# Performance work log

Hardware: AMD Instinct MI355X
Metric: run time of the kernel (lower is better)

The kernel has to match this reference:

```python
import jax, jax.numpy as jnp
import numpy as np

HEADS = 16
DIM_HEAD = 64
SCALE = DIM_HEAD ** -0.5
MASK_NEG = 1000000.0


def setup_inputs() -> dict:
    key = jax.random.key(0)
    ks = jax.random.split(key, 6)
    B, N, M, D = 2, 2048, 2048, 1024
    inner = HEADS * DIM_HEAD  # 1024
    x = jax.random.normal(ks[0], (B, N, D), dtype=jnp.float32)
    context = jax.random.normal(ks[1], (B, M, D), dtype=jnp.float32)
    mask = jax.random.randint(ks[2], (B, N), 0, 2, dtype=jnp.int32)
    Wq = jax.random.normal(ks[3], (D, inner), dtype=jnp.float32) * (D ** -0.5)
    Wkv = jax.random.normal(ks[4], (D, 2 * inner), dtype=jnp.float32) * (D ** -0.5)
    Wout = jax.random.normal(ks[5], (inner, D), dtype=jnp.float32) * (inner ** -0.5)
    bout = jnp.zeros((D,), dtype=jnp.float32)
    return {"x": x, "context": context, "mask": mask,
            "Wq": Wq, "Wkv": Wkv, "Wout": Wout, "bout": bout}


def _split_heads(t):
    # [b, n, (h d)] -> [b, h, n, d]
    b, n, _ = t.shape
    return t.reshape(b, n, HEADS, DIM_HEAD).transpose(0, 2, 1, 3)


def reference(x, context, mask, Wq, Wkv, Wout, bout):
    kv = context @ Wkv                      # [b, m, 2*inner]
    k, v = jnp.split(kv, 2, axis=-1)
    q = x @ Wq                              # [b, n, inner]
    q, k, v = _split_heads(q), _split_heads(k), _split_heads(v)
    dots = jnp.einsum('bhnd,bhmd->bhnm', q, k) * SCALE
    # mask is [b, n]: additive penalty per query row (faithful to source)
    dots = dots - (1.0 - mask.astype(jnp.float32))[:, None, :, None] * MASK_NEG
    attn = jax.nn.softmax(dots, axis=-1)
    out = jnp.einsum('bhnm,bhmd->bhnd', attn, v)  # [b, h, n, d]
    b, h, n, d = out.shape
    out = out.transpose(0, 2, 1, 3).reshape(b, n, h * d)
    return out @ Wout + bout
```

## Files before the change

### kernel.cpp

```cpp
#include <hip/hip_runtime.h>
#include <hip/hip_bf16.h>
#include <math.h>

#define BATCH   2
#define NQ      2048
#define NKV     2048
#define DMODEL  1024
#define HEADS   16
#define INNER   1024
#define KVCOLS  2048

typedef short bf16x8 __attribute__((ext_vector_type(8)));
typedef float f32x4  __attribute__((ext_vector_type(4)));

__device__ __forceinline__ short f2bf(float x) {
    __hip_bfloat16 h = __float2bfloat16(x);
    return *reinterpret_cast<short*>(&h);
}
__device__ __forceinline__ float bf2f(short h) {
    unsigned int u = ((unsigned int)(unsigned short)h) << 16;
    float f;
    __builtin_memcpy(&f, &u, 4);
    return f;
}
__device__ __forceinline__ void gl_lds16(const void* g, void* l) {
    __builtin_amdgcn_global_load_lds(
        (const __attribute__((address_space(1))) unsigned int*)g,
        (__attribute__((address_space(3))) unsigned int*)l, 16, 0, 0);
}
__device__ __forceinline__ int sw(int row, int chunk) {
    return row * 64 + ((chunk ^ (row & 7)) << 3);
}

__device__ __forceinline__ void split_chunk(const float* __restrict__ in,
                                            short* __restrict__ hi,
                                            short* __restrict__ lo, int id)
{
    const int i = (id * 256 + (int)threadIdx.x) * 4;
    float4 v = *(const float4*)(in + i);
    short4 h, l;
    h.x = f2bf(v.x); l.x = f2bf(v.x - bf2f(h.x));
    h.y = f2bf(v.y); l.y = f2bf(v.y - bf2f(h.y));
    h.z = f2bf(v.z); l.z = f2bf(v.z - bf2f(h.z));
    h.w = f2bf(v.w); l.w = f2bf(v.w - bf2f(h.w));
    *(short4*)(hi + i) = h;
    *(short4*)(lo + i) = l;
}

__device__ __forceinline__ void tile_transpose_split(
    const float* __restrict__ W, short* __restrict__ Wth, short* __restrict__ Wtl,
    int Kd, int Nd, int bx, int by, int split)
{
    __shared__ float t[32][33];
    const int lx = threadIdx.x & 31, ly = threadIdx.x >> 5;
    #pragma unroll
    for (int j = 0; j < 4; ++j)
        t[ly + j * 8][lx] = W[(size_t)(by * 32 + ly + j * 8) * Nd + bx * 32 + lx];
    __syncthreads();
    #pragma unroll
    for (int j = 0; j < 4; ++j) {
        const float v = t[lx][ly + j * 8];
        const short h = f2bf(v);
        const size_t idx = (size_t)(bx * 32 + ly + j * 8) * Kd + by * 32 + lx;
        Wth[idx] = h;
        if (split) Wtl[idx] = f2bf(v - bf2f(h));
    }
}

__global__ __launch_bounds__(256)
void prep_all(const float* __restrict__ x, const float* __restrict__ ctx,
              const float* __restrict__ Wq, const float* __restrict__ Wkv,
              const float* __restrict__ Wout,
              short* __restrict__ xh, short* __restrict__ xl,
              short* __restrict__ ch, short* __restrict__ cl,
              short* __restrict__ WqTh, short* __restrict__ WqTl,
              short* __restrict__ WkvTh, short* __restrict__ WkvTl,
              short* __restrict__ WoutT)
{
    const int id = blockIdx.x;
    if (id < 4096) {
        split_chunk(x, xh, xl, id);
    } else if (id < 8192) {
        split_chunk(ctx, ch, cl, id - 4096);
    } else {
        const int r = id - 8192;
        if (r < 1024)
            tile_transpose_split(Wq, WqTh, WqTl, 1024, 1024, r & 31, r >> 5, 1);
        else if (r < 3072)
            tile_transpose_split(Wkv, WkvTh, WkvTl, 1024, 2048, (r - 1024) & 63, (r - 1024) >> 6, 1);
        else
            tile_transpose_split(Wout, WoutT, nullptr, 1024, 1024, (r - 3072) & 31, (r - 3072) >> 5, 0);
    }
}

__global__ __launch_bounds__(256)
void qkv_gemm(const short* __restrict__ xh, const short* __restrict__ xl,
              const short* __restrict__ ch, const short* __restrict__ cl,
              const short* __restrict__ WqTh, const short* __restrict__ WqTl,
              const short* __restrict__ WkvTh, const short* __restrict__ WkvTl,
              short* __restrict__ qhp, short* __restrict__ qlp,
              short* __restrict__ khp, short* __restrict__ klp,
              short* __restrict__ vp)
{
    __shared__ short Ash[128 * 32];
    __shared__ short Asl[128 * 32];
    __shared__ short Bsh[128 * 32];
    __shared__ short Bsl[128 * 32];

    const int tid = threadIdx.x;
    const int z = blockIdx.z;
    const int m0 = blockIdx.y * 128, n0 = blockIdx.x * 128;
    const int w = tid >> 6, ln = tid & 63;
    const int wm = (w & 1) * 64, wn = (w >> 1) * 64;
    const int lr = ln & 15, lq = ln >> 4;
    const int terms = (z == 2) ? 1 : 3;

    const short* Ah  = (z == 0) ? xh : ch;
    const short* Al  = (z == 0) ? xl : cl;
    const short* Bth = (z == 0) ? WqTh : (z == 1 ? WkvTh : WkvTh + (size_t)1024 * 1024);
    const short* Btl = (z == 0) ? WqTl : WkvTl;

    f32x4 acc[4][4];
    #pragma unroll
    for (int mt = 0; mt < 4; ++mt)
        #pragma unroll
        for (int nt = 0; nt < 4; ++nt)
            #pragma unroll
            for (int r = 0; r < 4; ++r) acc[mt][nt][r] = 0.0f;

    for (int k0 = 0; k0 < 1024; k0 += 32) {
        __syncthreads();
        #pragma unroll
        for (int it = 0; it < 2; ++it) {
            const int f = it * 256 + tid;
            const int row = f >> 2, c = f & 3;
            const int cg = c ^ ((row >> 1) & 3);
            const size_t ao = (size_t)(m0 + row) * 1024 + k0 + cg * 8;
            const size_t bo = (size_t)(n0 + row) * 1024 + k0 + cg * 8;
            gl_lds16(Ah  + ao, Ash + f * 8);
            gl_lds16(Bth + bo, Bsh + f * 8);
            if (terms == 3) {
                gl_lds16(Al  + ao, Asl + f * 8);
                gl_lds16(Btl + bo, Bsl + f * 8);
            }
        }
        __syncthreads();

        bf16x8 ah[4], bh[4];
        #pragma unroll
        for (int t = 0; t < 4; ++t) {
            const int ar = wm + t * 16 + lr;
            const int br = wn + t * 16 + lr;
            ah[t] = *(const bf16x8*)(Ash + ar * 32 + ((lq ^ ((ar >> 1) & 3)) << 3));
            bh[t] = *(const bf16x8*)(Bsh + br * 32 + ((lq ^ ((br >> 1) & 3)) << 3));
        }
        #pragma unroll
        for (int mt = 0; mt < 4; ++mt)
            #pragma unroll
            for (int nt = 0; nt < 4; ++nt)
                acc[mt][nt] = __builtin_amdgcn_mfma_f32_16x16x32_bf16(
                    ah[mt], bh[nt], acc[mt][nt], 0, 0, 0);

        if (terms == 3) {
            bf16x8 al[4], bl[4];
            #pragma unroll
            for (int t = 0; t < 4; ++t) {
                const int ar = wm + t * 16 + lr;
                const int br = wn + t * 16 + lr;
                al[t] = *(const bf16x8*)(Asl + ar * 32 + ((lq ^ ((ar >> 1) & 3)) << 3));
                bl[t] = *(const bf16x8*)(Bsl + br * 32 + ((lq ^ ((br >> 1) & 3)) << 3));
            }
            #pragma unroll
            for (int mt = 0; mt < 4; ++mt)
                #pragma unroll
                for (int nt = 0; nt < 4; ++nt) {
                    acc[mt][nt] = __builtin_amdgcn_mfma_f32_16x16x32_bf16(
                        ah[mt], bl[nt], acc[mt][nt], 0, 0, 0);
                    acc[mt][nt] = __builtin_amdgcn_mfma_f32_16x16x32_bf16(
                        al[mt], bh[nt], acc[mt][nt], 0, 0, 0);
                }
        }
    }

    const float scale = (z == 0) ? 0.125f : 1.0f;
    short* Chi = (z == 0) ? qhp : (z == 1 ? khp : vp);
    short* Clo = (z == 0) ? qlp : klp;
    #pragma unroll
    for (int mt = 0; mt < 4; ++mt)
        #pragma unroll
        for (int nt = 0; nt < 4; ++nt)
            #pragma unroll
            for (int r = 0; r < 4; ++r) {
                const int row = m0 + wm + mt * 16 + lq * 4 + r;
                const int col = n0 + wn + nt * 16 + lr;
                const float v = acc[mt][nt][r] * scale;
                const short hh = f2bf(v);
                Chi[(size_t)row * 1024 + col] = hh;
                if (z != 2)
                    Clo[(size_t)row * 1024 + col] = f2bf(v - bf2f(hh));
            }
}

__global__ __launch_bounds__(256)
void gemm_out(const short* __restrict__ A, const short* __restrict__ Bt,
              float* __restrict__ C, const float* __restrict__ bias)
{
    __shared__ short As[128 * 64];
    __shared__ short Bs[64 * 64];
    const int tid = threadIdx.x;
    const int m0 = blockIdx.y * 128, n0 = blockIdx.x * 64;
    const int w = tid >> 6, ln = tid & 63;
    const int wm = (w & 1) * 64, wn = (w >> 1) * 32;
    const int lr = ln & 15, lq = ln >> 4;

    f32x4 acc[4][2];
    #pragma unroll
    for (int mt = 0; mt < 4; ++mt)
        #pragma unroll
        for (int nt = 0; nt < 2; ++nt)
            #pragma unroll
            for (int r = 0; r < 4; ++r) acc[mt][nt][r] = 0.0f;

    for (int k0 = 0; k0 < 1024; k0 += 64) {
        __syncthreads();
        #pragma unroll
        for (int it = 0; it < 4; ++it) {
            const int f = it * 256 + tid;
            const int row = f >> 3, c8 = f & 7;
            const int cg = c8 ^ (row & 7);
            gl_lds16(A + (size_t)(m0 + row) * 1024 + k0 + cg * 8, As + f * 8);
        }
        #pragma unroll
        for (int it = 0; it < 2; ++it) {
            const int f = it * 256 + tid;
            const int row = f >> 3, c8 = f & 7;
            const int cg = c8 ^ (row & 7);
            gl_lds16(Bt + (size_t)(n0 + row) * 1024 + k0 + cg * 8, Bs + f * 8);
        }
        __syncthreads();
        #pragma unroll
        for (int ks = 0; ks < 2; ++ks) {
            bf16x8 af[4], bfr[2];
            #pragma unroll
            for (int t = 0; t < 4; ++t) {
                const int ar = wm + t * 16 + lr;
                af[t] = *(const bf16x8*)(As + ar * 64 + (((ks * 4 + lq) ^ (ar & 7)) << 3));
            }
            #pragma unroll
            for (int t = 0; t < 2; ++t) {
                const int br = wn + t * 16 + lr;
                bfr[t] = *(const bf16x8*)(Bs + br * 64 + (((ks * 4 + lq) ^ (br & 7)) << 3));
            }
            #pragma unroll
            for (int mt = 0; mt < 4; ++mt)
                #pragma unroll
                for (int nt = 0; nt < 2; ++nt)
                    acc[mt][nt] = __builtin_amdgcn_mfma_f32_16x16x32_bf16(
                        af[mt], bfr[nt], acc[mt][nt], 0, 0, 0);
        }
    }
    #pragma unroll
    for (int mt = 0; mt < 4; ++mt)
        #pragma unroll
        for (int nt = 0; nt < 2; ++nt)
            #pragma unroll
            for (int r = 0; r < 4; ++r) {
                const int row = m0 + wm + mt * 16 + lq * 4 + r;
                const int col = n0 + wn + nt * 16 + lr;
                C[(size_t)row * 1024 + col] = acc[mt][nt][r] + bias[col];
            }
}

__global__ __launch_bounds__(512, 4)
void flash_v8(const short* __restrict__ qh, const short* __restrict__ ql,
              const short* __restrict__ kh, const short* __restrict__ kl,
              const short* __restrict__ vp, short* __restrict__ aob)
{
    const int qt = blockIdx.x, h = blockIdx.y, b = blockIdx.z;
    const int tid = threadIdx.x;
    const int w = tid >> 6, ln = tid & 63;
    const int lr = ln & 15, lq = ln >> 4;

    __shared__ short Kh[2 * 4096];
    __shared__ short Kl[2 * 4096];
    __shared__ short Vt[2 * 4096];
    __shared__ short Ps[128 * 64];

    const size_t qrow0 = (size_t)(b * NQ + qt * 128);

    bf16x8 aqh[2], aql[2];
    #pragma unroll
    for (int ks = 0; ks < 2; ++ks) {
        const size_t qoff = (qrow0 + w * 16 + lr) * INNER + h * 64 + ks * 32 + lq * 8;
        aqh[ks] = *(const bf16x8*)(qh + qoff);
        aql[ks] = *(const bf16x8*)(ql + qoff);
    }

    const int srow = tid >> 3, sc8 = tid & 7;
    const int kdst = sw(srow, sc8);
    const int idx = tid & 31, dg4 = (tid >> 5) * 4;
    const int vj  = (idx & 15) + ((idx >> 4) << 5);
    const int kp32 = (idx & 15) * 2 + (idx >> 4);
    int4 rkh, rkl; int2 rva, rvb;

    {
        const size_t koff = (size_t)(b * NKV + srow) * INNER + h * 64 + sc8 * 8;
        rkh = *(const int4*)(kh + koff);
        rkl = *(const int4*)(kl + koff);
        const short* v0 = vp + (size_t)(b * NKV + vj) * INNER + h * 64 + dg4;
        rva = *(const int2*)(v0);
        rvb = *(const int2*)(v0 + 16 * INNER);
        *(int4*)(Kh + kdst) = rkh;
        *(int4*)(Kl + kdst) = rkl;
        const short* as = (const short*)&rva;
        const short* bs = (const short*)&rvb;
        int* vt32 = (int*)Vt;
        #pragma unroll
        for (int j = 0; j < 4; ++j)
            vt32[(dg4 + j) * 32 + (((kp32 >> 2) ^ ((dg4 + j) & 7)) << 2) + (kp32 & 3)] =
                (int)((unsigned short)as[j] | ((unsigned int)(unsigned short)bs[j] << 16));
    }

    float psum[4];
    #pragma unroll
    for (int r = 0; r < 4; ++r) psum[r] = 0.0f;
    f32x4 oacc[4];
    #pragma unroll
    for (int dg = 0; dg < 4; ++dg)
        #pragma unroll
        for (int r = 0; r < 4; ++r) oacc[dg][r] = 0.0f;

    for (int kt = 0; kt < NKV / 64; ++kt) {
        const int cur = kt & 1;
        if (kt < NKV / 64 - 1) {
            const size_t krow0 = (size_t)(b * NKV + (kt + 1) * 64);
            const size_t koff = (krow0 + srow) * INNER + h * 64 + sc8 * 8;
            rkh = *(const int4*)(kh + koff);
            rkl = *(const int4*)(kl + koff);
            const short* v0 = vp + (krow0 + vj) * INNER + h * 64 + dg4;
            rva = *(const int2*)(v0);
            rvb = *(const int2*)(v0 + 16 * INNER);
        }
        __syncthreads();

        const short* KhC = Kh + cur * 4096;
        const short* KlC = Kl + cur * 4096;
        const short* VtC = Vt + cur * 4096;

        f32x4 sacc[4];
        #pragma unroll
        for (int g = 0; g < 4; ++g)
            #pragma unroll
            for (int r = 0; r < 4; ++r) sacc[g][r] = 0.0f;
        #pragma unroll
        for (int ks = 0; ks < 2; ++ks) {
            #pragma unroll
            for (int g = 0; g < 4; ++g) {
                const bf16x8 bkh = *(const bf16x8*)(KhC + sw(g * 16 + lr, ks * 4 + lq));
                const bf16x8 bkl = *(const bf16x8*)(KlC + sw(g * 16 + lr, ks * 4 + lq));
                sacc[g] = __builtin_amdgcn_mfma_f32_16x16x32_bf16(aqh[ks], bkh, sacc[g], 0, 0, 0);
                sacc[g] = __builtin_amdgcn_mfma_f32_16x16x32_bf16(aqh[ks], bkl, sacc[g], 0, 0, 0);
                sacc[g] = __builtin_amdgcn_mfma_f32_16x16x32_bf16(aql[ks], bkh, sacc[g], 0, 0, 0);
            }
        }

        #pragma unroll
        for (int r = 0; r < 4; ++r) {
            const int prow = w * 16 + lq * 4 + r;
            float pv[4];
            #pragma unroll
            for (int g = 0; g < 4; ++g) {
                pv[g] = __expf(sacc[g][r]);
                psum[r] += pv[g];
            }
            short4 pw;
            pw.x = f2bf(pv[0]); pw.y = f2bf(pv[1]);
            pw.z = f2bf(pv[2]); pw.w = f2bf(pv[3]);
            *(short4*)(Ps + sw(prow, lr >> 1) + (lr & 1) * 4) = pw;
        }

        #pragma unroll
        for (int ks = 0; ks < 2; ++ks) {
            const bf16x8 ap = *(const bf16x8*)(Ps + sw(w * 16 + lr, ks * 4 + lq));
            #pragma unroll
            for (int dg = 0; dg < 4; ++dg) {
                const bf16x8 bv = *(const bf16x8*)(VtC + sw(dg * 16 + lr, ks * 4 + lq));
                oacc[dg] = __builtin_amdgcn_mfma_f32_16x16x32_bf16(ap, bv, oacc[dg], 0, 0, 0);
            }
        }

        if (kt < NKV / 64 - 1) {
            short* KhN = Kh + (cur ^ 1) * 4096;
            short* KlN = Kl + (cur ^ 1) * 4096;
            *(int4*)(KhN + kdst) = rkh;
            *(int4*)(KlN + kdst) = rkl;
            const short* as = (const short*)&rva;
            const short* bs = (const short*)&rvb;
            int* vt32 = (int*)(Vt + (cur ^ 1) * 4096);
            #pragma unroll
            for (int j = 0; j < 4; ++j)
                vt32[(dg4 + j) * 32 + (((kp32 >> 2) ^ ((dg4 + j) & 7)) << 2) + (kp32 & 3)] =
                    (int)((unsigned short)as[j] | ((unsigned int)(unsigned short)bs[j] << 16));
        }
    }

    #pragma unroll
    for (int off = 1; off < 16; off <<= 1)
        #pragma unroll
        for (int r = 0; r < 4; ++r)
            psum[r] += __shfl_xor(psum[r], off, 64);

    #pragma unroll
    for (int dg = 0; dg < 4; ++dg)
        #pragma unroll
        for (int r = 0; r < 4; ++r) {
            const int row = w * 16 + lq * 4 + r;
            aob[(qrow0 + row) * INNER + h * 64 + dg * 16 + lr] =
                f2bf(oacc[dg][r] / psum[r]);
        }
}

extern "C" void kernel_launch(void* const* d_in, const int* in_sizes, int n_in,
                              void* d_out, int out_size, void* d_ws, size_t ws_size,
                              hipStream_t stream)
{
    const float* x    = (const float*)d_in[0];
    const float* ctx  = (const float*)d_in[1];
    const float* Wq   = (const float*)d_in[3];
    const float* Wkv  = (const float*)d_in[4];
    const float* Wout = (const float*)d_in[5];
    const float* bout = (const float*)d_in[6];
    float* out = (float*)d_out;

    short* base  = (short*)d_ws;
    short* xh    = base;
    short* xl    = base + (size_t)4 * 1024 * 1024;
    short* aob   = xh;
    short* WqTh  = base + (size_t) 8 * 1024 * 1024;
    short* WqTl  = base + (size_t) 9 * 1024 * 1024;
    short* qhp   = base + (size_t)10 * 1024 * 1024;
    short* qlp   = base + (size_t)14 * 1024 * 1024;
    short* WkvTh = base + (size_t)18 * 1024 * 1024;
    short* WkvTl = base + (size_t)20 * 1024 * 1024;
    short* khp   = base + (size_t)22 * 1024 * 1024;
    short* klp   = base + (size_t)26 * 1024 * 1024;
    short* WoutT = base + (size_t)30 * 1024 * 1024;
    short* ch    = base + (size_t)31 * 1024 * 1024;
    short* cl    = base + (size_t)35 * 1024 * 1024;
    short* vp    = base + (size_t)39 * 1024 * 1024;

    const dim3 blk(256);
    prep_all<<<12288, blk, 0, stream>>>(x, ctx, Wq, Wkv, Wout,
                                        xh, xl, ch, cl,
                                        WqTh, WqTl, WkvTh, WkvTl, WoutT);
    qkv_gemm<<<dim3(8, 32, 3), blk, 0, stream>>>(
        xh, xl, ch, cl, WqTh, WqTl, WkvTh, WkvTl,
        qhp, qlp, khp, klp, vp);
    flash_v8<<<dim3(NQ / 128, HEADS, BATCH), dim3(512), 0, stream>>>(
        qhp, qlp, khp, klp, vp, aob);
    gemm_out<<<dim3(1024 / 64, 4096 / 128), blk, 0, stream>>>(
        aob, WoutT, out, bout);
}
```

Before: 262.6 us.

## Split flash warps into row-group by key-half tiles with LDS partial reduction

Each of the eight warps now owns 32 query rows (two m-tiles) and half of each 64-key tile, instead of 16 rows across all 64 keys. Each K and V fragment read from shared memory therefore feeds two MFMAs, cutting LDS read traffic per MFMA. The V-transpose layout and P store pattern change to match the key split. The two key halves' output accumulators and row sums are combined through shared memory at the end, which costs extra registers, an extra barrier and some LDS traffic. The per-iteration barrier also moves to the top of the loop.

```diff
diff --git a/kernel.cpp b/kernel.cpp
--- a/kernel.cpp
+++ b/kernel.cpp
@@ -272,7 +272,7 @@
 }
 
 __global__ __launch_bounds__(512, 4)
-void flash_v8(const short* __restrict__ qh, const short* __restrict__ ql,
+void flash_v9(const short* __restrict__ qh, const short* __restrict__ ql,
               const short* __restrict__ kh, const short* __restrict__ kl,
               const short* __restrict__ vp, short* __restrict__ aob)
 {
@@ -280,6 +280,7 @@
     const int tid = threadIdx.x;
     const int w = tid >> 6, ln = tid & 63;
     const int lr = ln & 15, lq = ln >> 4;
+    const int rg = w >> 1, kh2 = w & 1;
 
     __shared__ short Kh[2 * 4096];
     __shared__ short Kl[2 * 4096];
@@ -288,19 +289,21 @@
 
     const size_t qrow0 = (size_t)(b * NQ + qt * 128);
 
-    bf16x8 aqh[2], aql[2];
-    #pragma unroll
-    for (int ks = 0; ks < 2; ++ks) {
-        const size_t qoff = (qrow0 + w * 16 + lr) * INNER + h * 64 + ks * 32 + lq * 8;
-        aqh[ks] = *(const bf16x8*)(qh + qoff);
-        aql[ks] = *(const bf16x8*)(ql + qoff);
-    }
+    bf16x8 aqh[2][2], aql[2][2];
+    #pragma unroll
+    for (int mt = 0; mt < 2; ++mt)
+        #pragma unroll
+        for (int ks = 0; ks < 2; ++ks) {
+            const size_t qoff = (qrow0 + rg * 32 + mt * 16 + lr) * INNER
+                              + h * 64 + ks * 32 + lq * 8;
+            aqh[mt][ks] = *(const bf16x8*)(qh + qoff);
+            aql[mt][ks] = *(const bf16x8*)(ql + qoff);
+        }
 
     const int srow = tid >> 3, sc8 = tid & 7;
     const int kdst = sw(srow, sc8);
     const int idx = tid & 31, dg4 = (tid >> 5) * 4;
     const int vj  = (idx & 15) + ((idx >> 4) << 5);
-    const int kp32 = (idx & 15) * 2 + (idx >> 4);
     int4 rkh, rkl; int2 rva, rvb;
 
     {
@@ -317,21 +320,27 @@
         int* vt32 = (int*)Vt;
         #pragma unroll
         for (int j = 0; j < 4; ++j)
-            vt32[(dg4 + j) * 32 + (((kp32 >> 2) ^ ((dg4 + j) & 7)) << 2) + (kp32 & 3)] =
+            vt32[(dg4 + j) * 32 + (((idx >> 2) ^ ((dg4 + j) & 7)) << 2) + (idx & 3)] =
                 (int)((unsigned short)as[j] | ((unsigned int)(unsigned short)bs[j] << 16));
     }
 
-    float psum[4];
-    #pragma unroll
-    for (int r = 0; r < 4; ++r) psum[r] = 0.0f;
-    f32x4 oacc[4];
-    #pragma unroll
-    for (int dg = 0; dg < 4; ++dg)
-        #pragma unroll
-        for (int r = 0; r < 4; ++r) oacc[dg][r] = 0.0f;
+    float psum[2][4];
+    #pragma unroll
+    for (int mt = 0; mt < 2; ++mt)
+        #pragma unroll
+        for (int r = 0; r < 4; ++r) psum[mt][r] = 0.0f;
+    f32x4 oacc[2][4];
+    #pragma unroll
+    for (int mt = 0; mt < 2; ++mt)
+        #pragma unroll
+        for (int dg = 0; dg < 4; ++dg)
+            #pragma unroll
+            for (int r = 0; r < 4; ++r) oacc[mt][dg][r] = 0.0f;
 
     for (int kt = 0; kt < NKV / 64; ++kt) {
         const int cur = kt & 1;
+        __syncthreads();
+
         if (kt < NKV / 64 - 1) {
             const size_t krow0 = (size_t)(b * NKV + (kt + 1) * 64);
             const size_t koff = (krow0 + srow) * INNER + h * 64 + sc8 * 8;
@@ -341,51 +350,63 @@
             rva = *(const int2*)(v0);
             rvb = *(const int2*)(v0 + 16 * INNER);
         }
-        __syncthreads();
 
         const short* KhC = Kh + cur * 4096;
         const short* KlC = Kl + cur * 4096;
         const short* VtC = Vt + cur * 4096;
 
-        f32x4 sacc[4];
-        #pragma unroll
-        for (int g = 0; g < 4; ++g)
-            #pragma unroll
-            for (int r = 0; r < 4; ++r) sacc[g][r] = 0.0f;
+        f32x4 sacc[2][2];
+        #pragma unroll
+        for (int mt = 0; mt < 2; ++mt)
+            #pragma unroll
+            for (int g = 0; g < 2; ++g)
+                #pragma unroll
+                for (int r = 0; r < 4; ++r) sacc[mt][g][r] = 0.0f;
         #pragma unroll
         for (int ks = 0; ks < 2; ++ks) {
             #pragma unroll
-            for (int g = 0; g < 4; ++g) {
-                const bf16x8 bkh = *(const bf16x8*)(KhC + sw(g * 16 + lr, ks * 4 + lq));
-                const bf16x8 bkl = *(const bf16x8*)(KlC + sw(g * 16 + lr, ks * 4 + lq));
-                sacc[g] = __builtin_amdgcn_mfma_f32_16x16x32_bf16(aqh[ks], bkh, sacc[g], 0, 0, 0);
-                sacc[g] = __builtin_amdgcn_mfma_f32_16x16x32_bf16(aqh[ks], bkl, sacc[g], 0, 0, 0);
-                sacc[g] = __builtin_amdgcn_mfma_f32_16x16x32_bf16(aql[ks], bkh, sacc[g], 0, 0, 0);
-            }
-        }
-
-        #pragma unroll
-        for (int r = 0; r < 4; ++r) {
-            const int prow = w * 16 + lq * 4 + r;
-            float pv[4];
-            #pragma unroll
-            for (int g = 0; g < 4; ++g) {
-                pv[g] = __expf(sacc[g][r]);
-                psum[r] += pv[g];
-            }
-            short4 pw;
-            pw.x = f2bf(pv[0]); pw.y = f2bf(pv[1]);
-            pw.z = f2bf(pv[2]); pw.w = f2bf(pv[3]);
-            *(short4*)(Ps + sw(prow, lr >> 1) + (lr & 1) * 4) = pw;
-        }
-
-        #pragma unroll
-        for (int ks = 0; ks < 2; ++ks) {
-            const bf16x8 ap = *(const bf16x8*)(Ps + sw(w * 16 + lr, ks * 4 + lq));
+            for (int g = 0; g < 2; ++g) {
+                const int krow = kh2 * 32 + g * 16 + lr;
+                const bf16x8 bkh = *(const bf16x8*)(KhC + sw(krow, ks * 4 + lq));
+                const bf16x8 bkl = *(const bf16x8*)(KlC + sw(krow, ks * 4 + lq));
+                #pragma unroll
+                for (int mt = 0; mt < 2; ++mt) {
+                    sacc[mt][g] = __builtin_amdgcn_mfma_f32_16x16x32_bf16(
+                        aqh[mt][ks], bkh, sacc[mt][g], 0, 0, 0);
+                    sacc[mt][g] = __builtin_amdgcn_mfma_f32_16x16x32_bf16(
+                        aqh[mt][ks], bkl, sacc[mt][g], 0, 0, 0);
+                    sacc[mt][g] = __builtin_amdgcn_mfma_f32_16x16x32_bf16(
+                        aql[mt][ks], bkh, sacc[mt][g], 0, 0, 0);
+                }
+            }
+        }
+
+        #pragma unroll
+        for (int mt = 0; mt < 2; ++mt)
+            #pragma unroll
+            for (int r = 0; r < 4; ++r) {
+                const int prow = rg * 32 + mt * 16 + lq * 4 + r;
+                const float p0 = __expf(sacc[mt][0][r]);
+                const float p1 = __expf(sacc[mt][1][r]);
+                psum[mt][r] += p0 + p1;
+                const unsigned int pk =
+                    (unsigned int)(unsigned short)f2bf(p0) |
+                    ((unsigned int)(unsigned short)f2bf(p1) << 16);
+                *(unsigned int*)(Ps + sw(prow, kh2 * 4 + (lr >> 2)) + (lr & 3) * 2) = pk;
+            }
+
+        {
+            bf16x8 ap[2];
+            #pragma unroll
+            for (int mt = 0; mt < 2; ++mt)
+                ap[mt] = *(const bf16x8*)(Ps + sw(rg * 32 + mt * 16 + lr, kh2 * 4 + lq));
             #pragma unroll
             for (int dg = 0; dg < 4; ++dg) {
-                const bf16x8 bv = *(const bf16x8*)(VtC + sw(dg * 16 + lr, ks * 4 + lq));
-                oacc[dg] = __builtin_amdgcn_mfma_f32_16x16x32_bf16(ap, bv, oacc[dg], 0, 0, 0);
+                const bf16x8 bv = *(const bf16x8*)(VtC + sw(dg * 16 + lr, kh2 * 4 + lq));
+                #pragma unroll
+                for (int mt = 0; mt < 2; ++mt)
+                    oacc[mt][dg] = __builtin_amdgcn_mfma_f32_16x16x32_bf16(
+                        ap[mt], bv, oacc[mt][dg], 0, 0, 0);
             }
         }
 
@@ -399,25 +420,61 @@
             int* vt32 = (int*)(Vt + (cur ^ 1) * 4096);
             #pragma unroll
             for (int j = 0; j < 4; ++j)
-                vt32[(dg4 + j) * 32 + (((kp32 >> 2) ^ ((dg4 + j) & 7)) << 2) + (kp32 & 3)] =
+                vt32[(dg4 + j) * 32 + (((idx >> 2) ^ ((dg4 + j) & 7)) << 2) + (idx & 3)] =
                     (int)((unsigned short)as[j] | ((unsigned int)(unsigned short)bs[j] << 16));
         }
     }
 
-    #pragma unroll
-    for (int off = 1; off < 16; off <<= 1)
-        #pragma unroll
-        for (int r = 0; r < 4; ++r)
-            psum[r] += __shfl_xor(psum[r], off, 64);
-
-    #pragma unroll
-    for (int dg = 0; dg < 4; ++dg)
-        #pragma unroll
-        for (int r = 0; r < 4; ++r) {
-            const int row = w * 16 + lq * 4 + r;
-            aob[(qrow0 + row) * INNER + h * 64 + dg * 16 + lr] =
-                f2bf(oacc[dg][r] / psum[r]);
-        }
+    __syncthreads();
+    float* sc0 = (float*)Kh;
+    float* sc1 = (float*)Kl;
+    float* scp = (float*)Ps;
+    if (kh2 == 1) {
+        #pragma unroll
+        for (int dg = 0; dg < 4; ++dg)
+            #pragma unroll
+            for (int r = 0; r < 4; ++r) {
+                sc0[(dg * 4 + r) * 256 + rg * 64 + ln] = oacc[0][dg][r];
+                sc1[(dg * 4 + r) * 256 + rg * 64 + ln] = oacc[1][dg][r];
+            }
+        #pragma unroll
+        for (int mt = 0; mt < 2; ++mt)
+            #pragma unroll
+            for (int r = 0; r < 4; ++r)
+                scp[(mt * 4 + r) * 256 + rg * 64 + ln] = psum[mt][r];
+    }
+    __syncthreads();
+    if (kh2 == 0) {
+        #pragma unroll
+        for (int dg = 0; dg < 4; ++dg)
+            #pragma unroll
+            for (int r = 0; r < 4; ++r) {
+                oacc[0][dg][r] += sc0[(dg * 4 + r) * 256 + rg * 64 + ln];
+                oacc[1][dg][r] += sc1[(dg * 4 + r) * 256 + rg * 64 + ln];
+            }
+        #pragma unroll
+        for (int mt = 0; mt < 2; ++mt)
+            #pragma unroll
+            for (int r = 0; r < 4; ++r)
+                psum[mt][r] += scp[(mt * 4 + r) * 256 + rg * 64 + ln];
+        #pragma unroll
+        for (int off = 1; off < 16; off <<= 1)
+            #pragma unroll
+            for (int mt = 0; mt < 2; ++mt)
+                #pragma unroll
+                for (int r = 0; r < 4; ++r)
+                    psum[mt][r] += __shfl_xor(psum[mt][r], off, 64);
+        #pragma unroll
+        for (int mt = 0; mt < 2; ++mt)
+            #pragma unroll
+            for (int dg = 0; dg < 4; ++dg)
+                #pragma unroll
+                for (int r = 0; r < 4; ++r) {
+                    const int row = rg * 32 + mt * 16 + lq * 4 + r;
+                    aob[(qrow0 + row) * INNER + h * 64 + dg * 16 + lr] =
+                        f2bf(oacc[mt][dg][r] / psum[mt][r]);
+                }
+    }
 }
 
 extern "C" void kernel_launch(void* const* d_in, const int* in_sizes, int n_in,
@@ -456,7 +513,7 @@
     qkv_gemm<<<dim3(8, 32, 3), blk, 0, stream>>>(
         xh, xl, ch, cl, WqTh, WqTl, WkvTh, WkvTl,
         qhp, qlp, khp, klp, vp);
-    flash_v8<<<dim3(NQ / 128, HEADS, BATCH), dim3(512), 0, stream>>>(
+    flash_v9<<<dim3(NQ / 128, HEADS, BATCH), dim3(512), 0, stream>>>(
         qhp, qlp, khp, klp, vp, aob);
     gemm_out<<<dim3(1024 / 64, 4096 / 128), blk, 0, stream>>>(
         aob, WoutT, out, bout);
```

Measured after the change: 299.2 us. 13.9% more time.
